# Kernel optimization log

Measured on AMD Instinct MI355X. Metric: run time of the kernel, lower is better.

## Reference

```python
import jax, jax.numpy as jnp
import numpy as np

NUM_HEADS = 16

def setup_inputs() -> dict:
    key = jax.random.key(0)
    ks = jax.random.split(key, 5)
    B, S, H = 16, 1025, 1024
    std = 0.02
    return {
        "hidden_states": jax.random.normal(ks[0], (B, S, H), jnp.float32),
        "w_qkv": jax.random.normal(ks[1], (3 * H, H), jnp.float32) * std,
        "b_qkv": jax.random.normal(ks[2], (3 * H,), jnp.float32) * std,
        "w_dense": jax.random.normal(ks[3], (H, H), jnp.float32) * std,
        "b_dense": jax.random.normal(ks[4], (H,), jnp.float32) * std,
    }

def reference(hidden_states, w_qkv, b_qkv, w_dense, b_dense):
    B, S, H = hidden_states.shape
    nh = NUM_HEADS
    hd = H // nh
    scale = hd ** -0.5
    # fused QKV projection: [B,S,3H]
    mixed = jnp.einsum('bsh,oh->bso', hidden_states, w_qkv) + b_qkv
    # reshape per torch: (B,S,nh,3,hd) -> permute(3,0,2,1,4)
    mixed = mixed.reshape(B, S, nh, 3, hd).transpose(3, 0, 2, 1, 4)
    q, k, v = mixed[0], mixed[1], mixed[2]          # each [B,nh,S,hd]
    scores = jnp.einsum('bhqd,bhkd->bhqk', q, k) * scale
    probs = jax.nn.softmax(scores, axis=-1)          # [B,nh,S,S]
    ctx = jnp.einsum('bhqk,bhkd->bhqd', probs, v)    # [B,nh,S,hd]
    ctx = ctx.transpose(0, 2, 1, 3).reshape(B, S, H)
    out = jnp.einsum('bsh,oh->bso', ctx, w_dense) + b_dense
    return out
```

## Files before the change

kernel.cpp:

```cpp
#include <hip/hip_runtime.h>
#include <math.h>

typedef float f32x4 __attribute__((ext_vector_type(4)));
typedef __bf16 bf16x8 __attribute__((ext_vector_type(8)));
typedef unsigned int u32;
typedef u32 u32x4 __attribute__((ext_vector_type(4)));

#define AS1 __attribute__((address_space(1)))
#define AS3 __attribute__((address_space(3)))

static __device__ __forceinline__ void gload16(const void* g, void* l) {
    __builtin_amdgcn_global_load_lds((const AS1 u32*)g, (AS3 u32*)l, 16, 0, 0);
}
static __device__ __forceinline__ f32x4 mfma16(bf16x8 a, bf16x8 b, f32x4 c) {
    return __builtin_amdgcn_mfma_f32_16x16x32_bf16(a, b, c, 0, 0, 0);
}
static __device__ __forceinline__ float exp2fast(float x) {
    return __builtin_amdgcn_exp2f(x);
}

__global__ __launch_bounds__(256)
void convert3_kernel(const float* __restrict__ in0, __bf16* __restrict__ out0, int nb0,
                     const float* __restrict__ in1, __bf16* __restrict__ out1, int nb1,
                     const float* __restrict__ in2, __bf16* __restrict__ out2)
{
    int b = blockIdx.x;
    const float* in; __bf16* out;
    if (b < nb0)            { in = in0; out = out0; }
    else if (b < nb0 + nb1) { in = in1; out = out1; b -= nb0; }
    else                    { in = in2; out = out2; b -= nb0 + nb1; }
    const size_t i = ((size_t)b * 256 + threadIdx.x) * 8;
    f32x4 a = *(const f32x4*)(in + i);
    f32x4 c = *(const f32x4*)(in + i + 4);
    bf16x8 o;
    #pragma unroll
    for (int j = 0; j < 4; ++j) { o[j] = (__bf16)a[j]; o[j + 4] = (__bf16)c[j]; }
    *(bf16x8*)(out + i) = o;
}

template<int MODE>
__global__ __launch_bounds__(512)
void gemm_big(const __bf16* __restrict__ A, const __bf16* __restrict__ Bw,
              const float* __restrict__ bias, __bf16* __restrict__ qkv,
              float* __restrict__ f_out)
{
    constexpr int M = 16400;
    constexpr int K = 1024;
    constexpr int NBX = (MODE == 0) ? 24 : 8;
    constexpr int NOUT = (MODE == 0) ? 3072 : 1024;
    constexpr int CHUNK = (65 * NBX) / 8;

    __shared__ __align__(16) __bf16 As[256 * 64];
    __shared__ __align__(16) __bf16 Bs[128 * 64];

    const int tid  = threadIdx.x;
    const int lane = tid & 63;
    const int wv   = tid >> 6;
    const int wrm  = wv >> 1;
    const int wcn  = wv & 1;
    const int fr   = lane & 15, fq = lane >> 4;

    const int xx = blockIdx.x & 7, jj = blockIdx.x >> 3;
    const int tile = xx * CHUNK + jj;
    const int by = tile / NBX, bx = tile % NBX;
    const int m0 = by * 256, n0 = bx * 128;

    const __bf16* aptr[4]; int aoff[4];
    #pragma unroll
    for (int qd = 0; qd < 4; ++qd) {
        const int s = qd * 512 + tid;
        const int r = s >> 3;
        const int c = (s & 7) ^ (r & 7);
        aoff[qd] = s * 8;
        int ar = m0 + r; if (ar > M - 1) ar = M - 1;
        aptr[qd] = A + (size_t)ar * K + c * 8;
    }
    const __bf16* bptr[2]; int boff[2];
    #pragma unroll
    for (int l = 0; l < 2; ++l) {
        const int s = l * 512 + tid;
        const int r = s >> 3;
        const int c = (s & 7) ^ (r & 7);
        boff[l] = s * 8;
        bptr[l] = Bw + (size_t)(n0 + r) * K + c * 8;
    }

    f32x4 acc[4][4];
    #pragma unroll
    for (int i = 0; i < 4; ++i)
        #pragma unroll
        for (int j = 0; j < 4; ++j)
            acc[i][j] = f32x4{0.f, 0.f, 0.f, 0.f};

    for (int kt = 0; kt < K / 64; ++kt) {
        const int kof = kt * 64;
        #pragma unroll
        for (int qd = 0; qd < 4; ++qd) gload16(aptr[qd] + kof, &As[aoff[qd]]);
        #pragma unroll
        for (int l = 0; l < 2; ++l)   gload16(bptr[l] + kof, &Bs[boff[l]]);
        __syncthreads();

        #pragma unroll
        for (int ks = 0; ks < 2; ++ks) {
            bf16x8 a[4], b[4];
            #pragma unroll
            for (int i = 0; i < 4; ++i) {
                const int ra = wrm * 64 + i * 16 + fr;
                const int rb = wcn * 64 + i * 16 + fr;
                const int cga = ((ks * 4 + fq) ^ (ra & 7)) * 8;
                const int cgb = ((ks * 4 + fq) ^ (rb & 7)) * 8;
                a[i] = *(const bf16x8*)&As[ra * 64 + cga];
                b[i] = *(const bf16x8*)&Bs[rb * 64 + cgb];
            }
            #pragma unroll
            for (int i = 0; i < 4; ++i)
                #pragma unroll
                for (int j = 0; j < 4; ++j)
                    acc[i][j] = mfma16(a[i], b[j], acc[i][j]);
        }
        __syncthreads();
    }

    #pragma unroll
    for (int ni = 0; ni < 4; ++ni) {
        const int col = n0 + wcn * 64 + ni * 16 + fr;
        const float bv = bias[col];
        if constexpr (MODE == 0) {
            const float scale = ((col % 192) < 64) ? 0.18033688011112042f : 1.0f;
            #pragma unroll
            for (int mi = 0; mi < 4; ++mi) {
                #pragma unroll
                for (int j = 0; j < 4; ++j) {
                    const int m = m0 + wrm * 64 + mi * 16 + fq * 4 + j;
                    if (m < M)
                        qkv[(size_t)m * NOUT + col] =
                            (__bf16)((acc[mi][ni][j] + bv) * scale);
                }
            }
        } else {
            #pragma unroll
            for (int mi = 0; mi < 4; ++mi) {
                #pragma unroll
                for (int j = 0; j < 4; ++j) {
                    const int m = m0 + wrm * 64 + mi * 16 + fq * 4 + j;
                    if (m < M) f_out[(size_t)m * NOUT + col] = acc[mi][ni][j] + bv;
                }
            }
        }
    }
}

__global__ __launch_bounds__(256)
void transpose_v(const __bf16* __restrict__ qkvb, __bf16* __restrict__ vt)
{
    constexpr int S = 1025, S2 = 1088;
    const int bh = blockIdx.y;
    const int bb = bh >> 4, hh = bh & 15;
    const int s0 = blockIdx.x * 64;
    const int sr = threadIdx.x >> 2, sq = threadIdx.x & 3;
    int srow = s0 + sr; if (srow > S - 1) srow = S - 1;
    const __bf16* src = qkvb + ((size_t)(bb * 1025) + srow) * 3072
                             + hh * 192 + 128 + sq * 16;
    bf16x8 v0 = *(const bf16x8*)src;
    bf16x8 v1 = *(const bf16x8*)(src + 8);
    __bf16* dst = vt + (size_t)bh * 64 * S2 + s0 + sr;
    #pragma unroll
    for (int i = 0; i < 8; ++i) {
        dst[(size_t)(sq * 16 + i) * S2]     = v0[i];
        dst[(size_t)(sq * 16 + 8 + i) * S2] = v1[i];
    }
}

__global__ __launch_bounds__(512)
void attn_kernel(const __bf16* __restrict__ qkvb, const __bf16* __restrict__ vtb,
                 __bf16* __restrict__ ctxb)
{
    constexpr int S = 1025, S2 = 1088, ROW = 3072;
    const int tid  = threadIdx.x;
    const int lane = tid & 63;
    const int w    = tid >> 6;
    const int fr   = lane & 15, fq = lane >> 4;

    const int xx = blockIdx.x & 7, jj = blockIdx.x >> 3;
    const int tile = xx * 288 + jj;
    const int bh = tile / 9;
    const int q0 = (tile % 9) * 128;
    const int bb = bh >> 4, hh = bh & 15;

    const __bf16* qp = qkvb + (size_t)(bb * 1025) * ROW + hh * 192;
    const __bf16* kp = qp + 64;
    const __bf16* vp = vtb + (size_t)bh * 64 * S2;

    __shared__ __align__(16) __bf16 Ks[64 * 64];
    __shared__ __align__(16) __bf16 Vs[64 * 64];
    __shared__ u32 Ps[8][16 * 33];

    const int r0 = tid >> 3, g0 = (tid & 7) ^ ((tid >> 3) & 7);

    int qrow = q0 + w * 16 + fr; if (qrow > S - 1) qrow = S - 1;
    const bf16x8 qa0 = *(const bf16x8*)(qp + (size_t)qrow * ROW + fq * 8);
    const bf16x8 qa1 = *(const bf16x8*)(qp + (size_t)qrow * ROW + 32 + fq * 8);

    f32x4 ctx[4];
    #pragma unroll
    for (int di = 0; di < 4; ++di) ctx[di] = f32x4{0.f, 0.f, 0.f, 0.f};
    float mrow = -1e30f;
    float lrow = 0.f;

    u32* psrow_w = &Ps[w][fr * 33];

    for (int kt = 0; kt < 17; ++kt) {
        const int kv0 = kt * 64;
        {
            int kr = kv0 + r0; if (kr > S - 1) kr = S - 1;
            gload16(kp + (size_t)kr * ROW + g0 * 8, &Ks[tid * 8]);
            gload16(vp + (size_t)r0 * S2 + kv0 + g0 * 8, &Vs[tid * 8]);
        }
        __syncthreads();

        f32x4 sc[4];
        #pragma unroll
        for (int ni = 0; ni < 4; ++ni) {
            const int row = ni * 16 + fr;
            bf16x8 kf0 = *(const bf16x8*)&Ks[row * 64 + ((fq    ) ^ (row & 7)) * 8];
            bf16x8 kf1 = *(const bf16x8*)&Ks[row * 64 + ((fq + 4) ^ (row & 7)) * 8];
            f32x4 z = f32x4{0.f, 0.f, 0.f, 0.f};
            z = mfma16(kf0, qa0, z);
            sc[ni] = mfma16(kf1, qa1, z);
        }
        if (kv0 + 64 > S) {
            #pragma unroll
            for (int ni = 0; ni < 4; ++ni)
                #pragma unroll
                for (int j = 0; j < 4; ++j)
                    if (kv0 + ni * 16 + fq * 4 + j >= S) sc[ni][j] = -1e30f;
        }

        float mt = sc[0][0];
        #pragma unroll
        for (int ni = 0; ni < 4; ++ni)
            #pragma unroll
            for (int j = 0; j < 4; ++j) mt = fmaxf(mt, sc[ni][j]);
        mt = fmaxf(mt, __shfl_xor(mt, 16, 64));
        mt = fmaxf(mt, __shfl_xor(mt, 32, 64));

        if (__any(mt > mrow + 8.0f)) {
            const float mnew = fmaxf(mrow, mt);
            const float alpha = exp2fast(mrow - mnew);
            mrow = mnew;
            lrow *= alpha;
            float av[4];
            #pragma unroll
            for (int j = 0; j < 4; ++j) av[j] = __shfl(alpha, fq * 4 + j, 64);
            #pragma unroll
            for (int di = 0; di < 4; ++di) {
                ctx[di][0] *= av[0]; ctx[di][1] *= av[1];
                ctx[di][2] *= av[2]; ctx[di][3] *= av[3];
            }
        }

        float p[4][4];
        float s = 0.f;
        #pragma unroll
        for (int ni = 0; ni < 4; ++ni)
            #pragma unroll
            for (int j = 0; j < 4; ++j) {
                p[ni][j] = exp2fast(sc[ni][j] - mrow);
                s += p[ni][j];
            }
        s += __shfl_xor(s, 16, 64);
        s += __shfl_xor(s, 32, 64);
        lrow += s;

        #pragma unroll
        for (int ni = 0; ni < 4; ++ni) {
            #pragma unroll
            for (int h = 0; h < 2; ++h) {
                unsigned short lo = __builtin_bit_cast(unsigned short, (__bf16)p[ni][2 * h]);
                unsigned short hi = __builtin_bit_cast(unsigned short, (__bf16)p[ni][2 * h + 1]);
                psrow_w[fq * 8 + ni * 2 + h] = (u32)lo | ((u32)hi << 16);
            }
        }
        u32x4 pav[2];
        #pragma unroll
        for (int ks = 0; ks < 2; ++ks)
            #pragma unroll
            for (int t = 0; t < 4; ++t) {
                const int slot = (2 * (fq & 1) + (t >> 1)) * 8
                               + (2 * ks + (fq >> 1)) * 2 + (t & 1);
                pav[ks][t] = psrow_w[slot];
            }

        #pragma unroll
        for (int ks = 0; ks < 2; ++ks) {
            const bf16x8 pa = __builtin_bit_cast(bf16x8, pav[ks]);
            #pragma unroll
            for (int di = 0; di < 4; ++di) {
                const int row = di * 16 + fr;
                bf16x8 vf = *(const bf16x8*)&Vs[row * 64 + ((ks * 4 + fq) ^ (row & 7)) * 8];
                ctx[di] = mfma16(pa, vf, ctx[di]);
            }
        }
        __syncthreads();
    }

    float linv[4];
    #pragma unroll
    for (int j = 0; j < 4; ++j) linv[j] = 1.0f / __shfl(lrow, fq * 4 + j, 64);
    #pragma unroll
    for (int di = 0; di < 4; ++di) {
        #pragma unroll
        for (int j = 0; j < 4; ++j) {
            const int qg = q0 + w * 16 + fq * 4 + j;
            if (qg < S) {
                ctxb[((size_t)bb * 1025 + qg) * 1024 + hh * 64 + di * 16 + fr] =
                    (__bf16)(ctx[di][j] * linv[j]);
            }
        }
    }
}

extern "C" void kernel_launch(void* const* d_in, const int* in_sizes, int n_in,
                              void* d_out, int out_size, void* d_ws, size_t ws_size,
                              hipStream_t stream)
{
    const float* hs      = (const float*)d_in[0];
    const float* w_qkv   = (const float*)d_in[1];
    const float* b_qkv   = (const float*)d_in[2];
    const float* w_dense = (const float*)d_in[3];
    const float* b_dense = (const float*)d_in[4];

    const size_t nHS  = (size_t)16 * 1025 * 1024;
    const size_t nWQ  = (size_t)3072 * 1024;
    const size_t nWD  = (size_t)1024 * 1024;
    const size_t nQKV = (size_t)16400 * 3072;

    __bf16* hsb     = (__bf16*)d_ws;
    __bf16* wqkvb   = hsb + nHS;
    __bf16* wdenseb = wqkvb + nWQ;
    __bf16* qkvb    = wdenseb + nWD;
    __bf16* ctxb    = qkvb + nQKV;
    __bf16* vtb     = ctxb + nHS;

    convert3_kernel<<<dim3(8200 + 1536 + 512), dim3(256), 0, stream>>>(
        hs, hsb, 8200, w_qkv, wqkvb, 1536, w_dense, wdenseb);

    gemm_big<0><<<dim3(65 * 24), dim3(512), 0, stream>>>(
        hsb, wqkvb, b_qkv, qkvb, nullptr);

    transpose_v<<<dim3(17, 256), dim3(256), 0, stream>>>(qkvb, vtb);

    attn_kernel<<<dim3(8 * 288), dim3(512), 0, stream>>>(qkvb, vtb, ctxb);

    gemm_big<1><<<dim3(65 * 8), dim3(512), 0, stream>>>(
        ctxb, wdenseb, b_dense, nullptr, (float*)d_out);
}
```

Before: 389.7 us.

## Double-buffer QKV GEMM and write V transposed from its epilogue

The QKV projection GEMM now uses a two-stage LDS double buffer with 32-wide K slices. The next tile's global-to-LDS loads are issued before computing the current one, with partial vmcnt waits and raised MFMA priority. Its epilogue writes the V columns directly into the transposed [b,h,d,s] buffer, which removes the separate transpose_v kernel launch and its extra read and write of V. The cost is scattered 2-byte strided stores for the V part of the epilogue, and the dense GEMM is split out as its own non-template kernel.

```diff
diff --git a/kernel.cpp b/kernel.cpp
--- a/kernel.cpp
+++ b/kernel.cpp
@@ -38,16 +38,138 @@
     *(bf16x8*)(out + i) = o;
 }
 
-template<int MODE>
 __global__ __launch_bounds__(512)
-void gemm_big(const __bf16* __restrict__ A, const __bf16* __restrict__ Bw,
-              const float* __restrict__ bias, __bf16* __restrict__ qkv,
-              float* __restrict__ f_out)
+void gemm_qkv_p2(const __bf16* __restrict__ A, const __bf16* __restrict__ Bw,
+                 const float* __restrict__ bias, __bf16* __restrict__ qkv,
+                 __bf16* __restrict__ vt)
 {
     constexpr int M = 16400;
     constexpr int K = 1024;
-    constexpr int NBX = (MODE == 0) ? 24 : 8;
-    constexpr int NOUT = (MODE == 0) ? 3072 : 1024;
+    constexpr int NST = 32;
+    constexpr int NBX = 24;
+    constexpr int CHUNK = (65 * NBX) / 8;
+
+    __shared__ __align__(16) __bf16 As[2][256 * 32];
+    __shared__ __align__(16) __bf16 Bs[2][128 * 32];
+
+    const int tid  = threadIdx.x;
+    const int lane = tid & 63;
+    const int wv   = tid >> 6;
+    const int wrm  = wv >> 1;
+    const int wcn  = wv & 1;
+    const int fr   = lane & 15, fq = lane >> 4;
+
+    const int xx = blockIdx.x & 7, jj = blockIdx.x >> 3;
+    const int tile = xx * CHUNK + jj;
+    const int by = tile / NBX, bx = tile % NBX;
+    const int m0 = by * 256, n0 = bx * 128;
+
+    const __bf16* aptr[2]; int aoff[2];
+    #pragma unroll
+    for (int l = 0; l < 2; ++l) {
+        const int s = l * 512 + tid;
+        const int r = s >> 2;
+        const int c = (s & 3) ^ (r & 3);
+        aoff[l] = s * 8;
+        int ar = m0 + r; if (ar > M - 1) ar = M - 1;
+        aptr[l] = A + (size_t)ar * K + c * 8;
+    }
+    const __bf16* bptr; int boff;
+    {
+        const int s = tid;
+        const int r = s >> 2;
+        const int c = (s & 3) ^ (r & 3);
+        boff = s * 8;
+        bptr = Bw + (size_t)(n0 + r) * K + c * 8;
+    }
+
+#define STAGE(nb, ko) { \
+    gload16(aptr[0] + (ko), &As[nb][aoff[0]]); \
+    gload16(aptr[1] + (ko), &As[nb][aoff[1]]); \
+    gload16(bptr    + (ko), &Bs[nb][boff]);    }
+
+    f32x4 acc[4][4];
+    #pragma unroll
+    for (int i = 0; i < 4; ++i)
+        #pragma unroll
+        for (int j = 0; j < 4; ++j)
+            acc[i][j] = f32x4{0.f, 0.f, 0.f, 0.f};
+
+    STAGE(0, 0);
+
+    for (int t = 0; t < NST; ++t) {
+        const int cur = t & 1;
+        if (t + 1 < NST) {
+            STAGE(cur ^ 1, (t + 1) * 32);
+            asm volatile("s_waitcnt vmcnt(3)" ::: "memory");
+        } else {
+            asm volatile("s_waitcnt vmcnt(0)" ::: "memory");
+        }
+        __builtin_amdgcn_s_barrier();
+
+        bf16x8 a[4], b[4];
+        #pragma unroll
+        for (int i = 0; i < 4; ++i) {
+            const int ra = wrm * 64 + i * 16 + fr;
+            const int rb = wcn * 64 + i * 16 + fr;
+            a[i] = *(const bf16x8*)&As[cur][ra * 32 + ((fq ^ (ra & 3)) * 8)];
+            b[i] = *(const bf16x8*)&Bs[cur][rb * 32 + ((fq ^ (rb & 3)) * 8)];
+        }
+        __builtin_amdgcn_s_setprio(1);
+        #pragma unroll
+        for (int i = 0; i < 4; ++i)
+            #pragma unroll
+            for (int j = 0; j < 4; ++j)
+                acc[i][j] = mfma16(a[i], b[j], acc[i][j]);
+        __builtin_amdgcn_s_setprio(0);
+        __builtin_amdgcn_s_barrier();
+    }
+
+    #pragma unroll
+    for (int ni = 0; ni < 4; ++ni) {
+        const int col = n0 + wcn * 64 + ni * 16 + fr;
+        const float bv = bias[col];
+        const int tsel = (col >> 6) % 3;
+        if (tsel < 2) {
+            const float scale = (tsel == 0) ? 0.18033688011112042f : 1.0f;
+            #pragma unroll
+            for (int mi = 0; mi < 4; ++mi) {
+                #pragma unroll
+                for (int j = 0; j < 4; ++j) {
+                    const int m = m0 + wrm * 64 + mi * 16 + fq * 4 + j;
+                    if (m < M)
+                        qkv[(size_t)m * 3072 + col] =
+                            (__bf16)((acc[mi][ni][j] + bv) * scale);
+                }
+            }
+        } else {
+            const int head = col / 192;
+            const int d    = col & 63;
+            #pragma unroll
+            for (int mi = 0; mi < 4; ++mi) {
+                #pragma unroll
+                for (int j = 0; j < 4; ++j) {
+                    const int m = m0 + wrm * 64 + mi * 16 + fq * 4 + j;
+                    if (m < M) {
+                        const int bb = m / 1025;
+                        const int ss = m - bb * 1025;
+                        vt[((size_t)((bb * 16 + head) * 64 + d)) * 1088 + ss] =
+                            (__bf16)(acc[mi][ni][j] + bv);
+                    }
+                }
+            }
+        }
+    }
+#undef STAGE
+}
+
+__global__ __launch_bounds__(512)
+void gemm_dense(const __bf16* __restrict__ A, const __bf16* __restrict__ Bw,
+                const float* __restrict__ bias, float* __restrict__ f_out)
+{
+    constexpr int M = 16400;
+    constexpr int K = 1024;
+    constexpr int NBX = 8;
     constexpr int CHUNK = (65 * NBX) / 8;
 
     __shared__ __align__(16) __bf16 As[256 * 64];
@@ -107,10 +229,8 @@
             for (int i = 0; i < 4; ++i) {
                 const int ra = wrm * 64 + i * 16 + fr;
                 const int rb = wcn * 64 + i * 16 + fr;
-                const int cga = ((ks * 4 + fq) ^ (ra & 7)) * 8;
-                const int cgb = ((ks * 4 + fq) ^ (rb & 7)) * 8;
-                a[i] = *(const bf16x8*)&As[ra * 64 + cga];
-                b[i] = *(const bf16x8*)&Bs[rb * 64 + cgb];
+                a[i] = *(const bf16x8*)&As[ra * 64 + ((ks * 4 + fq) ^ (ra & 7)) * 8];
+                b[i] = *(const bf16x8*)&Bs[rb * 64 + ((ks * 4 + fq) ^ (rb & 7)) * 8];
             }
             #pragma unroll
             for (int i = 0; i < 4; ++i)
@@ -125,49 +245,14 @@
     for (int ni = 0; ni < 4; ++ni) {
         const int col = n0 + wcn * 64 + ni * 16 + fr;
         const float bv = bias[col];
-        if constexpr (MODE == 0) {
-            const float scale = ((col % 192) < 64) ? 0.18033688011112042f : 1.0f;
-            #pragma unroll
-            for (int mi = 0; mi < 4; ++mi) {
-                #pragma unroll
-                for (int j = 0; j < 4; ++j) {
-                    const int m = m0 + wrm * 64 + mi * 16 + fq * 4 + j;
-                    if (m < M)
-                        qkv[(size_t)m * NOUT + col] =
-                            (__bf16)((acc[mi][ni][j] + bv) * scale);
-                }
-            }
-        } else {
-            #pragma unroll
-            for (int mi = 0; mi < 4; ++mi) {
-                #pragma unroll
-                for (int j = 0; j < 4; ++j) {
-                    const int m = m0 + wrm * 64 + mi * 16 + fq * 4 + j;
-                    if (m < M) f_out[(size_t)m * NOUT + col] = acc[mi][ni][j] + bv;
-                }
-            }
-        }
-    }
-}
-
-__global__ __launch_bounds__(256)
-void transpose_v(const __bf16* __restrict__ qkvb, __bf16* __restrict__ vt)
-{
-    constexpr int S = 1025, S2 = 1088;
-    const int bh = blockIdx.y;
-    const int bb = bh >> 4, hh = bh & 15;
-    const int s0 = blockIdx.x * 64;
-    const int sr = threadIdx.x >> 2, sq = threadIdx.x & 3;
-    int srow = s0 + sr; if (srow > S - 1) srow = S - 1;
-    const __bf16* src = qkvb + ((size_t)(bb * 1025) + srow) * 3072
-                             + hh * 192 + 128 + sq * 16;
-    bf16x8 v0 = *(const bf16x8*)src;
-    bf16x8 v1 = *(const bf16x8*)(src + 8);
-    __bf16* dst = vt + (size_t)bh * 64 * S2 + s0 + sr;
-    #pragma unroll
-    for (int i = 0; i < 8; ++i) {
-        dst[(size_t)(sq * 16 + i) * S2]     = v0[i];
-        dst[(size_t)(sq * 16 + 8 + i) * S2] = v1[i];
+        #pragma unroll
+        for (int mi = 0; mi < 4; ++mi) {
+            #pragma unroll
+            for (int j = 0; j < 4; ++j) {
+                const int m = m0 + wrm * 64 + mi * 16 + fq * 4 + j;
+                if (m < M) f_out[(size_t)m * 1024 + col] = acc[mi][ni][j] + bv;
+            }
+        }
     }
 }
 
@@ -345,13 +430,11 @@
     convert3_kernel<<<dim3(8200 + 1536 + 512), dim3(256), 0, stream>>>(
         hs, hsb, 8200, w_qkv, wqkvb, 1536, w_dense, wdenseb);
 
-    gemm_big<0><<<dim3(65 * 24), dim3(512), 0, stream>>>(
-        hsb, wqkvb, b_qkv, qkvb, nullptr);
-
-    transpose_v<<<dim3(17, 256), dim3(256), 0, stream>>>(qkvb, vtb);
+    gemm_qkv_p2<<<dim3(65 * 24), dim3(512), 0, stream>>>(
+        hsb, wqkvb, b_qkv, qkvb, vtb);
 
     attn_kernel<<<dim3(8 * 288), dim3(512), 0, stream>>>(qkvb, vtb, ctxb);
 
-    gemm_big<1><<<dim3(65 * 8), dim3(512), 0, stream>>>(
-        ctxb, wdenseb, b_dense, nullptr, (float*)d_out);
-}
+    gemm_dense<<<dim3(65 * 8), dim3(512), 0, stream>>>(
+        ctxb, wdenseb, b_dense, (float*)d_out);
+}
```

Result: no change. 397.1 us (+1.9%).

## Widen GEMM tiles to 256x256 and fuse V transpose into QKV epilogue

Applied to the files above, without the earlier changes.

The GEMM block tile grows from 256x128 to 256x256: each A tile loaded into shared memory is reused against two B sub-tiles, which halves A traffic and the number of workgroups. The QKV GEMM epilogue now writes V directly in transposed layout, so the separate transpose_v kernel and its extra read and write of V are gone. In exchange, doubled accumulators raise register pressure (launch bounds force one block per CU), the transposed V stores are strided and uncoalesced, and fewer workgroups may leave CUs underused, especially for the dense GEMM with only 260 blocks.

```diff
diff --git a/kernel.cpp b/kernel.cpp
--- a/kernel.cpp
+++ b/kernel.cpp
@@ -39,19 +39,20 @@
 }
 
 template<int MODE>
-__global__ __launch_bounds__(512)
-void gemm_big(const __bf16* __restrict__ A, const __bf16* __restrict__ Bw,
+__global__ __launch_bounds__(512, 1)
+void gemm_nb2(const __bf16* __restrict__ A, const __bf16* __restrict__ Bw,
               const float* __restrict__ bias, __bf16* __restrict__ qkv,
-              float* __restrict__ f_out)
+              __bf16* __restrict__ vt, float* __restrict__ f_out)
 {
     constexpr int M = 16400;
     constexpr int K = 1024;
-    constexpr int NBX = (MODE == 0) ? 24 : 8;
+    constexpr int NBXP = (MODE == 0) ? 6 : 2;
+    constexpr int NBP  = (MODE == 0) ? 12 : 4;
+    constexpr int NWG  = 65 * NBP;
     constexpr int NOUT = (MODE == 0) ? 3072 : 1024;
-    constexpr int CHUNK = (65 * NBX) / 8;
 
     __shared__ __align__(16) __bf16 As[256 * 64];
-    __shared__ __align__(16) __bf16 Bs[128 * 64];
+    __shared__ __align__(16) __bf16 Bs[2][128 * 64];
 
     const int tid  = threadIdx.x;
     const int lane = tid & 63;
@@ -60,10 +61,15 @@
     const int wcn  = wv & 1;
     const int fr   = lane & 15, fq = lane >> 4;
 
-    const int xx = blockIdx.x & 7, jj = blockIdx.x >> 3;
-    const int tile = xx * CHUNK + jj;
-    const int by = tile / NBX, bx = tile % NBX;
-    const int m0 = by * 256, n0 = bx * 128;
+    int tile;
+    {
+        const int Q = NWG / 8, R = NWG % 8;
+        const int x = blockIdx.x & 7, j = blockIdx.x >> 3;
+        tile = (x < R ? x * (Q + 1) : R * (Q + 1) + (x - R) * Q) + j;
+    }
+    const int by = tile / NBP, bxp = tile % NBP;
+    const int m0 = by * 256, n0 = bxp * 256;
+    (void)NBXP;
 
     const __bf16* aptr[4]; int aoff[4];
     #pragma unroll
@@ -75,99 +81,112 @@
         int ar = m0 + r; if (ar > M - 1) ar = M - 1;
         aptr[qd] = A + (size_t)ar * K + c * 8;
     }
-    const __bf16* bptr[2]; int boff[2];
+    const __bf16* bptr[2][2]; int boff[2];
     #pragma unroll
     for (int l = 0; l < 2; ++l) {
         const int s = l * 512 + tid;
         const int r = s >> 3;
         const int c = (s & 7) ^ (r & 7);
         boff[l] = s * 8;
-        bptr[l] = Bw + (size_t)(n0 + r) * K + c * 8;
-    }
-
-    f32x4 acc[4][4];
-    #pragma unroll
-    for (int i = 0; i < 4; ++i)
-        #pragma unroll
-        for (int j = 0; j < 4; ++j)
-            acc[i][j] = f32x4{0.f, 0.f, 0.f, 0.f};
+        #pragma unroll
+        for (int p = 0; p < 2; ++p)
+            bptr[p][l] = Bw + (size_t)(n0 + p * 128 + r) * K + c * 8;
+    }
+
+    f32x4 acc[2][4][4];
+    #pragma unroll
+    for (int p = 0; p < 2; ++p)
+        #pragma unroll
+        for (int i = 0; i < 4; ++i)
+            #pragma unroll
+            for (int j = 0; j < 4; ++j)
+                acc[p][i][j] = f32x4{0.f, 0.f, 0.f, 0.f};
 
     for (int kt = 0; kt < K / 64; ++kt) {
         const int kof = kt * 64;
         #pragma unroll
         for (int qd = 0; qd < 4; ++qd) gload16(aptr[qd] + kof, &As[aoff[qd]]);
         #pragma unroll
-        for (int l = 0; l < 2; ++l)   gload16(bptr[l] + kof, &Bs[boff[l]]);
+        for (int p = 0; p < 2; ++p)
+            #pragma unroll
+            for (int l = 0; l < 2; ++l)
+                gload16(bptr[p][l] + kof, &Bs[p][boff[l]]);
         __syncthreads();
 
         #pragma unroll
         for (int ks = 0; ks < 2; ++ks) {
-            bf16x8 a[4], b[4];
+            bf16x8 a[4];
             #pragma unroll
             for (int i = 0; i < 4; ++i) {
                 const int ra = wrm * 64 + i * 16 + fr;
-                const int rb = wcn * 64 + i * 16 + fr;
-                const int cga = ((ks * 4 + fq) ^ (ra & 7)) * 8;
-                const int cgb = ((ks * 4 + fq) ^ (rb & 7)) * 8;
-                a[i] = *(const bf16x8*)&As[ra * 64 + cga];
-                b[i] = *(const bf16x8*)&Bs[rb * 64 + cgb];
-            }
-            #pragma unroll
-            for (int i = 0; i < 4; ++i)
+                a[i] = *(const bf16x8*)&As[ra * 64 + ((ks * 4 + fq) ^ (ra & 7)) * 8];
+            }
+            #pragma unroll
+            for (int p = 0; p < 2; ++p) {
+                bf16x8 b[4];
                 #pragma unroll
-                for (int j = 0; j < 4; ++j)
-                    acc[i][j] = mfma16(a[i], b[j], acc[i][j]);
+                for (int i = 0; i < 4; ++i) {
+                    const int rb = wcn * 64 + i * 16 + fr;
+                    b[i] = *(const bf16x8*)&Bs[p][rb * 64 + ((ks * 4 + fq) ^ (rb & 7)) * 8];
+                }
+                #pragma unroll
+                for (int i = 0; i < 4; ++i)
+                    #pragma unroll
+                    for (int j = 0; j < 4; ++j)
+                        acc[p][i][j] = mfma16(a[i], b[j], acc[p][i][j]);
+            }
         }
         __syncthreads();
     }
 
     #pragma unroll
-    for (int ni = 0; ni < 4; ++ni) {
-        const int col = n0 + wcn * 64 + ni * 16 + fr;
-        const float bv = bias[col];
-        if constexpr (MODE == 0) {
-            const float scale = ((col % 192) < 64) ? 0.18033688011112042f : 1.0f;
-            #pragma unroll
-            for (int mi = 0; mi < 4; ++mi) {
+    for (int p = 0; p < 2; ++p) {
+        #pragma unroll
+        for (int ni = 0; ni < 4; ++ni) {
+            const int col = n0 + p * 128 + wcn * 64 + ni * 16 + fr;
+            const float bv = bias[col];
+            if constexpr (MODE == 0) {
+                const int tsel = (col >> 6) % 3;
+                if (tsel < 2) {
+                    const float scale = (tsel == 0) ? 0.18033688011112042f : 1.0f;
+                    #pragma unroll
+                    for (int mi = 0; mi < 4; ++mi) {
+                        #pragma unroll
+                        for (int j = 0; j < 4; ++j) {
+                            const int m = m0 + wrm * 64 + mi * 16 + fq * 4 + j;
+                            if (m < M)
+                                qkv[(size_t)m * 3072 + col] =
+                                    (__bf16)((acc[p][mi][ni][j] + bv) * scale);
+                        }
+                    }
+                } else {
+                    const int head = col / 192;
+                    const int d    = col & 63;
+                    #pragma unroll
+                    for (int mi = 0; mi < 4; ++mi) {
+                        #pragma unroll
+                        for (int j = 0; j < 4; ++j) {
+                            const int m = m0 + wrm * 64 + mi * 16 + fq * 4 + j;
+                            if (m < M) {
+                                const int bb = m / 1025;
+                                const int ss = m - bb * 1025;
+                                vt[((size_t)((bb * 16 + head) * 64 + d)) * 1088 + ss] =
+                                    (__bf16)(acc[p][mi][ni][j] + bv);
+                            }
+                        }
+                    }
+                }
+            } else {
                 #pragma unroll
-                for (int j = 0; j < 4; ++j) {
-                    const int m = m0 + wrm * 64 + mi * 16 + fq * 4 + j;
-                    if (m < M)
-                        qkv[(size_t)m * NOUT + col] =
-                            (__bf16)((acc[mi][ni][j] + bv) * scale);
+                for (int mi = 0; mi < 4; ++mi) {
+                    #pragma unroll
+                    for (int j = 0; j < 4; ++j) {
+                        const int m = m0 + wrm * 64 + mi * 16 + fq * 4 + j;
+                        if (m < M) f_out[(size_t)m * NOUT + col] = acc[p][mi][ni][j] + bv;
+                    }
                 }
             }
-        } else {
-            #pragma unroll
-            for (int mi = 0; mi < 4; ++mi) {
-                #pragma unroll
-                for (int j = 0; j < 4; ++j) {
-                    const int m = m0 + wrm * 64 + mi * 16 + fq * 4 + j;
-                    if (m < M) f_out[(size_t)m * NOUT + col] = acc[mi][ni][j] + bv;
-                }
-            }
-        }
-    }
-}
-
-__global__ __launch_bounds__(256)
-void transpose_v(const __bf16* __restrict__ qkvb, __bf16* __restrict__ vt)
-{
-    constexpr int S = 1025, S2 = 1088;
-    const int bh = blockIdx.y;
-    const int bb = bh >> 4, hh = bh & 15;
-    const int s0 = blockIdx.x * 64;
-    const int sr = threadIdx.x >> 2, sq = threadIdx.x & 3;
-    int srow = s0 + sr; if (srow > S - 1) srow = S - 1;
-    const __bf16* src = qkvb + ((size_t)(bb * 1025) + srow) * 3072
-                             + hh * 192 + 128 + sq * 16;
-    bf16x8 v0 = *(const bf16x8*)src;
-    bf16x8 v1 = *(const bf16x8*)(src + 8);
-    __bf16* dst = vt + (size_t)bh * 64 * S2 + s0 + sr;
-    #pragma unroll
-    for (int i = 0; i < 8; ++i) {
-        dst[(size_t)(sq * 16 + i) * S2]     = v0[i];
-        dst[(size_t)(sq * 16 + 8 + i) * S2] = v1[i];
+        }
     }
 }
 
@@ -345,13 +364,11 @@
     convert3_kernel<<<dim3(8200 + 1536 + 512), dim3(256), 0, stream>>>(
         hs, hsb, 8200, w_qkv, wqkvb, 1536, w_dense, wdenseb);
 
-    gemm_big<0><<<dim3(65 * 24), dim3(512), 0, stream>>>(
-        hsb, wqkvb, b_qkv, qkvb, nullptr);
-
-    transpose_v<<<dim3(17, 256), dim3(256), 0, stream>>>(qkvb, vtb);
+    gemm_nb2<0><<<dim3(65 * 12), dim3(512), 0, stream>>>(
+        hsb, wqkvb, b_qkv, qkvb, vtb, nullptr);
 
     attn_kernel<<<dim3(8 * 288), dim3(512), 0, stream>>>(qkvb, vtb, ctxb);
 
-    gemm_big<1><<<dim3(65 * 8), dim3(512), 0, stream>>>(
-        ctxb, wdenseb, b_dense, nullptr, (float*)d_out);
-}
+    gemm_nb2<1><<<dim3(65 * 4), dim3(512), 0, stream>>>(
+        ctxb, wdenseb, b_dense, nullptr, nullptr, (float*)d_out);
+}
```

Result: slower. 436.2 us (+11.9%).

## Fuse V transpose into QKV GEMM epilogue and double query rows per attention warp

Applied to the files above, without the earlier changes.

The QKV GEMM epilogue now writes the V slice straight into the transposed [B,heads,64,S] buffer, so the separate transpose_v kernel and its extra read of V are gone. The attention kernel now gives each warp two 16-row query tiles (256 query rows per block), so every K/V tile staged in LDS is reused across twice as many queries and the grid shrinks. The trade-offs: the V stores are scattered 2-byte writes, the 256-row tiling wastes more padded rows at the sequence tail, and the bigger per-warp state raises register pressure. The padding columns of the transposed V buffer (positions 1025 to 1087) are no longer written, so leftover workspace contents reach the P·V MFMAs wherever the masked probabilities are zero.

```diff
diff --git a/kernel.cpp b/kernel.cpp
--- a/kernel.cpp
+++ b/kernel.cpp
@@ -42,7 +42,7 @@
 __global__ __launch_bounds__(512)
 void gemm_big(const __bf16* __restrict__ A, const __bf16* __restrict__ Bw,
               const float* __restrict__ bias, __bf16* __restrict__ qkv,
-              float* __restrict__ f_out)
+              __bf16* __restrict__ vt, float* __restrict__ f_out)
 {
     constexpr int M = 16400;
     constexpr int K = 1024;
@@ -107,10 +107,8 @@
             for (int i = 0; i < 4; ++i) {
                 const int ra = wrm * 64 + i * 16 + fr;
                 const int rb = wcn * 64 + i * 16 + fr;
-                const int cga = ((ks * 4 + fq) ^ (ra & 7)) * 8;
-                const int cgb = ((ks * 4 + fq) ^ (rb & 7)) * 8;
-                a[i] = *(const bf16x8*)&As[ra * 64 + cga];
-                b[i] = *(const bf16x8*)&Bs[rb * 64 + cgb];
+                a[i] = *(const bf16x8*)&As[ra * 64 + ((ks * 4 + fq) ^ (ra & 7)) * 8];
+                b[i] = *(const bf16x8*)&Bs[rb * 64 + ((ks * 4 + fq) ^ (rb & 7)) * 8];
             }
             #pragma unroll
             for (int i = 0; i < 4; ++i)
@@ -126,15 +124,34 @@
         const int col = n0 + wcn * 64 + ni * 16 + fr;
         const float bv = bias[col];
         if constexpr (MODE == 0) {
-            const float scale = ((col % 192) < 64) ? 0.18033688011112042f : 1.0f;
-            #pragma unroll
-            for (int mi = 0; mi < 4; ++mi) {
-                #pragma unroll
-                for (int j = 0; j < 4; ++j) {
-                    const int m = m0 + wrm * 64 + mi * 16 + fq * 4 + j;
-                    if (m < M)
-                        qkv[(size_t)m * NOUT + col] =
-                            (__bf16)((acc[mi][ni][j] + bv) * scale);
+            const int tsel = (col >> 6) % 3;
+            if (tsel < 2) {
+                const float scale = (tsel == 0) ? 0.18033688011112042f : 1.0f;
+                #pragma unroll
+                for (int mi = 0; mi < 4; ++mi) {
+                    #pragma unroll
+                    for (int j = 0; j < 4; ++j) {
+                        const int m = m0 + wrm * 64 + mi * 16 + fq * 4 + j;
+                        if (m < M)
+                            qkv[(size_t)m * 3072 + col] =
+                                (__bf16)((acc[mi][ni][j] + bv) * scale);
+                    }
+                }
+            } else {
+                const int head = col / 192;
+                const int d    = col & 63;
+                #pragma unroll
+                for (int mi = 0; mi < 4; ++mi) {
+                    #pragma unroll
+                    for (int j = 0; j < 4; ++j) {
+                        const int m = m0 + wrm * 64 + mi * 16 + fq * 4 + j;
+                        if (m < M) {
+                            const int bb = m / 1025;
+                            const int ss = m - bb * 1025;
+                            vt[((size_t)((bb * 16 + head) * 64 + d)) * 1088 + ss] =
+                                (__bf16)(acc[mi][ni][j] + bv);
+                        }
+                    }
                 }
             }
         } else {
@@ -147,27 +164,6 @@
                 }
             }
         }
-    }
-}
-
-__global__ __launch_bounds__(256)
-void transpose_v(const __bf16* __restrict__ qkvb, __bf16* __restrict__ vt)
-{
-    constexpr int S = 1025, S2 = 1088;
-    const int bh = blockIdx.y;
-    const int bb = bh >> 4, hh = bh & 15;
-    const int s0 = blockIdx.x * 64;
-    const int sr = threadIdx.x >> 2, sq = threadIdx.x & 3;
-    int srow = s0 + sr; if (srow > S - 1) srow = S - 1;
-    const __bf16* src = qkvb + ((size_t)(bb * 1025) + srow) * 3072
-                             + hh * 192 + 128 + sq * 16;
-    bf16x8 v0 = *(const bf16x8*)src;
-    bf16x8 v1 = *(const bf16x8*)(src + 8);
-    __bf16* dst = vt + (size_t)bh * 64 * S2 + s0 + sr;
-    #pragma unroll
-    for (int i = 0; i < 8; ++i) {
-        dst[(size_t)(sq * 16 + i) * S2]     = v0[i];
-        dst[(size_t)(sq * 16 + 8 + i) * S2] = v1[i];
     }
 }
 
@@ -182,9 +178,9 @@
     const int fr   = lane & 15, fq = lane >> 4;
 
     const int xx = blockIdx.x & 7, jj = blockIdx.x >> 3;
-    const int tile = xx * 288 + jj;
-    const int bh = tile / 9;
-    const int q0 = (tile % 9) * 128;
+    const int tile = xx * 160 + jj;
+    const int bh = tile / 5;
+    const int q0 = (tile % 5) * 256;
     const int bb = bh >> 4, hh = bh & 15;
 
     const __bf16* qp = qkvb + (size_t)(bb * 1025) * ROW + hh * 192;
@@ -197,15 +193,21 @@
 
     const int r0 = tid >> 3, g0 = (tid & 7) ^ ((tid >> 3) & 7);
 
-    int qrow = q0 + w * 16 + fr; if (qrow > S - 1) qrow = S - 1;
-    const bf16x8 qa0 = *(const bf16x8*)(qp + (size_t)qrow * ROW + fq * 8);
-    const bf16x8 qa1 = *(const bf16x8*)(qp + (size_t)qrow * ROW + 32 + fq * 8);
-
-    f32x4 ctx[4];
-    #pragma unroll
-    for (int di = 0; di < 4; ++di) ctx[di] = f32x4{0.f, 0.f, 0.f, 0.f};
-    float mrow = -1e30f;
-    float lrow = 0.f;
+    bf16x8 qa[2][2];
+    #pragma unroll
+    for (int u = 0; u < 2; ++u) {
+        int qrow = q0 + w * 32 + u * 16 + fr; if (qrow > S - 1) qrow = S - 1;
+        qa[u][0] = *(const bf16x8*)(qp + (size_t)qrow * ROW + fq * 8);
+        qa[u][1] = *(const bf16x8*)(qp + (size_t)qrow * ROW + 32 + fq * 8);
+    }
+
+    f32x4 ctx[2][4];
+    #pragma unroll
+    for (int u = 0; u < 2; ++u)
+        #pragma unroll
+        for (int di = 0; di < 4; ++di) ctx[u][di] = f32x4{0.f, 0.f, 0.f, 0.f};
+    float mrow[2] = {-1e30f, -1e30f};
+    float lrow[2] = {0.f, 0.f};
 
     u32* psrow_w = &Ps[w][fr * 33];
 
@@ -218,103 +220,114 @@
         }
         __syncthreads();
 
-        f32x4 sc[4];
+        f32x4 sc[2][4];
         #pragma unroll
         for (int ni = 0; ni < 4; ++ni) {
             const int row = ni * 16 + fr;
             bf16x8 kf0 = *(const bf16x8*)&Ks[row * 64 + ((fq    ) ^ (row & 7)) * 8];
             bf16x8 kf1 = *(const bf16x8*)&Ks[row * 64 + ((fq + 4) ^ (row & 7)) * 8];
-            f32x4 z = f32x4{0.f, 0.f, 0.f, 0.f};
-            z = mfma16(kf0, qa0, z);
-            sc[ni] = mfma16(kf1, qa1, z);
+            #pragma unroll
+            for (int u = 0; u < 2; ++u) {
+                f32x4 z = f32x4{0.f, 0.f, 0.f, 0.f};
+                z = mfma16(kf0, qa[u][0], z);
+                sc[u][ni] = mfma16(kf1, qa[u][1], z);
+            }
         }
         if (kv0 + 64 > S) {
             #pragma unroll
             for (int ni = 0; ni < 4; ++ni)
                 #pragma unroll
                 for (int j = 0; j < 4; ++j)
-                    if (kv0 + ni * 16 + fq * 4 + j >= S) sc[ni][j] = -1e30f;
-        }
-
-        float mt = sc[0][0];
-        #pragma unroll
-        for (int ni = 0; ni < 4; ++ni)
-            #pragma unroll
-            for (int j = 0; j < 4; ++j) mt = fmaxf(mt, sc[ni][j]);
-        mt = fmaxf(mt, __shfl_xor(mt, 16, 64));
-        mt = fmaxf(mt, __shfl_xor(mt, 32, 64));
-
-        if (__any(mt > mrow + 8.0f)) {
-            const float mnew = fmaxf(mrow, mt);
-            const float alpha = exp2fast(mrow - mnew);
-            mrow = mnew;
-            lrow *= alpha;
-            float av[4];
-            #pragma unroll
-            for (int j = 0; j < 4; ++j) av[j] = __shfl(alpha, fq * 4 + j, 64);
-            #pragma unroll
-            for (int di = 0; di < 4; ++di) {
-                ctx[di][0] *= av[0]; ctx[di][1] *= av[1];
-                ctx[di][2] *= av[2]; ctx[di][3] *= av[3];
-            }
-        }
-
-        float p[4][4];
-        float s = 0.f;
-        #pragma unroll
-        for (int ni = 0; ni < 4; ++ni)
+                    if (kv0 + ni * 16 + fq * 4 + j >= S) {
+                        sc[0][ni][j] = -1e30f; sc[1][ni][j] = -1e30f;
+                    }
+        }
+
+        #pragma unroll
+        for (int u = 0; u < 2; ++u) {
+            float mt = sc[u][0][0];
+            #pragma unroll
+            for (int ni = 0; ni < 4; ++ni)
+                #pragma unroll
+                for (int j = 0; j < 4; ++j) mt = fmaxf(mt, sc[u][ni][j]);
+            mt = fmaxf(mt, __shfl_xor(mt, 16, 64));
+            mt = fmaxf(mt, __shfl_xor(mt, 32, 64));
+
+            if (__any(mt > mrow[u] + 8.0f)) {
+                const float mnew = fmaxf(mrow[u], mt);
+                const float alpha = exp2fast(mrow[u] - mnew);
+                mrow[u] = mnew;
+                lrow[u] *= alpha;
+                float av[4];
+                #pragma unroll
+                for (int j = 0; j < 4; ++j) av[j] = __shfl(alpha, fq * 4 + j, 64);
+                #pragma unroll
+                for (int di = 0; di < 4; ++di) {
+                    ctx[u][di][0] *= av[0]; ctx[u][di][1] *= av[1];
+                    ctx[u][di][2] *= av[2]; ctx[u][di][3] *= av[3];
+                }
+            }
+
+            float p[4][4];
+            float s = 0.f;
+            #pragma unroll
+            for (int ni = 0; ni < 4; ++ni)
+                #pragma unroll
+                for (int j = 0; j < 4; ++j) {
+                    p[ni][j] = exp2fast(sc[u][ni][j] - mrow[u]);
+                    s += p[ni][j];
+                }
+            s += __shfl_xor(s, 16, 64);
+            s += __shfl_xor(s, 32, 64);
+            lrow[u] += s;
+
+            #pragma unroll
+            for (int ni = 0; ni < 4; ++ni) {
+                #pragma unroll
+                for (int h = 0; h < 2; ++h) {
+                    unsigned short lo = __builtin_bit_cast(unsigned short, (__bf16)p[ni][2 * h]);
+                    unsigned short hi = __builtin_bit_cast(unsigned short, (__bf16)p[ni][2 * h + 1]);
+                    psrow_w[fq * 8 + ni * 2 + h] = (u32)lo | ((u32)hi << 16);
+                }
+            }
+            u32x4 pav[2];
+            #pragma unroll
+            for (int ks = 0; ks < 2; ++ks)
+                #pragma unroll
+                for (int t = 0; t < 4; ++t) {
+                    const int slot = (2 * (fq & 1) + (t >> 1)) * 8
+                                   + (2 * ks + (fq >> 1)) * 2 + (t & 1);
+                    pav[ks][t] = psrow_w[slot];
+                }
+
+            #pragma unroll
+            for (int ks = 0; ks < 2; ++ks) {
+                const bf16x8 pa = __builtin_bit_cast(bf16x8, pav[ks]);
+                #pragma unroll
+                for (int di = 0; di < 4; ++di) {
+                    const int row = di * 16 + fr;
+                    bf16x8 vf = *(const bf16x8*)&Vs[row * 64 + ((ks * 4 + fq) ^ (row & 7)) * 8];
+                    ctx[u][di] = mfma16(pa, vf, ctx[u][di]);
+                }
+            }
+        }
+        __syncthreads();
+    }
+
+    #pragma unroll
+    for (int u = 0; u < 2; ++u) {
+        float linv[4];
+        #pragma unroll
+        for (int j = 0; j < 4; ++j) linv[j] = 1.0f / __shfl(lrow[u], fq * 4 + j, 64);
+        #pragma unroll
+        for (int di = 0; di < 4; ++di) {
             #pragma unroll
             for (int j = 0; j < 4; ++j) {
-                p[ni][j] = exp2fast(sc[ni][j] - mrow);
-                s += p[ni][j];
-            }
-        s += __shfl_xor(s, 16, 64);
-        s += __shfl_xor(s, 32, 64);
-        lrow += s;
-
-        #pragma unroll
-        for (int ni = 0; ni < 4; ++ni) {
-            #pragma unroll
-            for (int h = 0; h < 2; ++h) {
-                unsigned short lo = __builtin_bit_cast(unsigned short, (__bf16)p[ni][2 * h]);
-                unsigned short hi = __builtin_bit_cast(unsigned short, (__bf16)p[ni][2 * h + 1]);
-                psrow_w[fq * 8 + ni * 2 + h] = (u32)lo | ((u32)hi << 16);
-            }
-        }
-        u32x4 pav[2];
-        #pragma unroll
-        for (int ks = 0; ks < 2; ++ks)
-            #pragma unroll
-            for (int t = 0; t < 4; ++t) {
-                const int slot = (2 * (fq & 1) + (t >> 1)) * 8
-                               + (2 * ks + (fq >> 1)) * 2 + (t & 1);
-                pav[ks][t] = psrow_w[slot];
-            }
-
-        #pragma unroll
-        for (int ks = 0; ks < 2; ++ks) {
-            const bf16x8 pa = __builtin_bit_cast(bf16x8, pav[ks]);
-            #pragma unroll
-            for (int di = 0; di < 4; ++di) {
-                const int row = di * 16 + fr;
-                bf16x8 vf = *(const bf16x8*)&Vs[row * 64 + ((ks * 4 + fq) ^ (row & 7)) * 8];
-                ctx[di] = mfma16(pa, vf, ctx[di]);
-            }
-        }
-        __syncthreads();
-    }
-
-    float linv[4];
-    #pragma unroll
-    for (int j = 0; j < 4; ++j) linv[j] = 1.0f / __shfl(lrow, fq * 4 + j, 64);
-    #pragma unroll
-    for (int di = 0; di < 4; ++di) {
-        #pragma unroll
-        for (int j = 0; j < 4; ++j) {
-            const int qg = q0 + w * 16 + fq * 4 + j;
-            if (qg < S) {
-                ctxb[((size_t)bb * 1025 + qg) * 1024 + hh * 64 + di * 16 + fr] =
-                    (__bf16)(ctx[di][j] * linv[j]);
+                const int qg = q0 + w * 32 + u * 16 + fq * 4 + j;
+                if (qg < S) {
+                    ctxb[((size_t)bb * 1025 + qg) * 1024 + hh * 64 + di * 16 + fr] =
+                        (__bf16)(ctx[u][di][j] * linv[j]);
+                }
             }
         }
     }
@@ -346,12 +359,10 @@
         hs, hsb, 8200, w_qkv, wqkvb, 1536, w_dense, wdenseb);
 
     gemm_big<0><<<dim3(65 * 24), dim3(512), 0, stream>>>(
-        hsb, wqkvb, b_qkv, qkvb, nullptr);
-
-    transpose_v<<<dim3(17, 256), dim3(256), 0, stream>>>(qkvb, vtb);
-
-    attn_kernel<<<dim3(8 * 288), dim3(512), 0, stream>>>(qkvb, vtb, ctxb);
+        hsb, wqkvb, b_qkv, qkvb, vtb, nullptr);
+
+    attn_kernel<<<dim3(8 * 160), dim3(512), 0, stream>>>(qkvb, vtb, ctxb);
 
     gemm_big<1><<<dim3(65 * 8), dim3(512), 0, stream>>>(
-        ctxb, wdenseb, b_dense, nullptr, (float*)d_out);
-}
+        ctxb, wdenseb, b_dense, nullptr, nullptr, (float*)d_out);
+}
```

Measured after the change: 390.4 us. Within noise of the previous version (+0.2%).
